# Optimization experiments

Measured on AMD Instinct MI355X. Metric: run time of the kernel, lower is better.

## Reference

```python
import jax, jax.numpy as jnp
import numpy as np

N = 100_000          # nodes
G = 2_000            # graphs
MUL0, MUL1 = 256, 128
DIM = MUL0 + 3 * MUL1  # 640
EPS = 1e-5
SQRT_K0 = 1.0 / np.sqrt(MUL0 + MUL1)          # fan_in of 0e slice: 256+128
SQRT_K1 = 1.0 / np.sqrt(MUL0 + 2 * MUL1)      # fan_in of 1e slice: 256+128+128


def setup_inputs() -> dict:
    key = jax.random.key(0)
    ks = jax.random.split(key, 8)
    x = jax.random.normal(ks[0], (N, DIM), dtype=jnp.float32)
    y = jax.random.normal(ks[1], (N, 4), dtype=jnp.float32)
    batch = jnp.sort(jax.random.randint(ks[2], (N,), 0, G)).astype(jnp.int32)
    # uvw path weights (e3nn internal weights, randn then rescaled by sqrt_k)
    w000 = jax.random.normal(ks[3], (MUL0, 1, MUL0), dtype=jnp.float32) * SQRT_K0
    w110 = jax.random.normal(ks[4], (MUL1, 1, MUL0), dtype=jnp.float32) * SQRT_K0
    w011 = jax.random.normal(ks[5], (MUL0, 1, MUL1), dtype=jnp.float32) * SQRT_K1
    w101 = jax.random.normal(ks[6], (MUL1, 1, MUL1), dtype=jnp.float32) * SQRT_K1
    w111 = jax.random.normal(ks[7], (MUL1, 1, MUL1), dtype=jnp.float32) * SQRT_K1
    bias0 = jnp.zeros((MUL0,), jnp.float32)           # bias on 0e slice
    mean_shift = jnp.ones((MUL0,), jnp.float32)
    affine_weight = jnp.ones((MUL0 + MUL1,), jnp.float32)
    affine_bias = jnp.zeros((MUL0,), jnp.float32)
    return dict(x=x, y=y, w000=w000, w011=w011, w101=w101, w110=w110,
                w111=w111, bias0=bias0, mean_shift=mean_shift,
                affine_weight=affine_weight, affine_bias=affine_bias,
                batch=batch)


def _segment_mean(vals, batch, counts):
    s = jax.ops.segment_sum(vals, batch, num_segments=G)
    return s / counts.reshape((G,) + (1,) * (vals.ndim - 1))


def reference(x, y, w000, w011, w101, w110, w111, bias0, mean_shift,
              affine_weight, affine_bias, batch):
    n = x.shape[0]
    s1 = x[:, :MUL0]                      # [N,256]  0e
    v1 = x[:, MUL0:].reshape(n, MUL1, 3)  # [N,128,3] 1e
    s2 = y[:, :1]                         # [N,1]    0e
    v2 = y[:, 1:].reshape(n, 1, 3)        # [N,1,3]  1e

    inv_sqrt3 = np.float32(1.0 / np.sqrt(3.0))
    # ---- fully connected tensor product (5 uvw paths) ----
    # output 0e slice: path weight sqrt(d_out)=1
    p000 = jnp.einsum('nu,nv,uvw->nw', s1, s2, w000)
    p110 = jnp.einsum('nui,nvi,uvw->nw', v1, v2, w110) * inv_sqrt3
    out0 = p000 + p110 + bias0                          # bias on scalar-even slice
    # output 1e slice: path weight sqrt(3); CG = 1/sqrt(3) (delta) or 1/sqrt(6) (eps)
    p011 = jnp.einsum('nu,nvk,uvw->nwk', s1, v2, w011)  # sqrt3/sqrt3 = 1
    p101 = jnp.einsum('nui,nv,uvw->nwi', v1, s2, w101)
    cross = jnp.cross(v1, v2)                           # [N,128,3]
    p111 = jnp.einsum('nuk,uvw->nwk', cross, w111) * np.float32(1.0 / np.sqrt(2.0))
    out1 = p011 + p101 + p111                           # [N,128,3]

    counts = jnp.maximum(
        jax.ops.segment_sum(jnp.ones((n,), x.dtype), batch, num_segments=G), 1.0)

    # ---- EquivariantGraphNorm (component norm, mean reduce, affine) ----
    # 0e field: per-graph mean shift, then per-graph rms normalization
    f0_mean = _segment_mean(out0, batch, counts)        # [G,256]
    f0 = out0 - f0_mean[batch] * mean_shift
    n0 = _segment_mean(f0 * f0, batch, counts)          # d=1 component norm
    n0 = jax.lax.rsqrt(n0 + EPS) * affine_weight[:MUL0]
    f0 = f0 * n0[batch] + affine_bias

    # 1e field: component norm = mean over the 3 components
    n1 = _segment_mean(jnp.mean(out1 * out1, axis=-1), batch, counts)  # [G,128]
    n1 = jax.lax.rsqrt(n1 + EPS) * affine_weight[MUL0:]
    f1 = out1 * n1[batch][:, :, None]

    return jnp.concatenate([f0, f1.reshape(n, MUL1 * 3)], axis=-1)
```

## Files before the change

kernel.cpp:

```cpp
#include <hip/hip_runtime.h>
#include <math.h>

#define N_ROWS 100000
#define NG     2000
#define M0     256
#define M1     128
#define DIMX   640
#define EPSV   1e-5f
#define BM     32

#define INV_SQRT3 0.57735026918962576f
#define INV_SQRT2 0.70710678118654752f

#define OFF_U  0
#define OFF_D  98304
#define OFF_V  131072
#define WT_TOTAL 163840

typedef __attribute__((ext_vector_type(8))) short bf16x8;
typedef __attribute__((ext_vector_type(4))) float f32x4;

__device__ __forceinline__ unsigned short f2bf(float f) {
    union { float f; unsigned int u; } v; v.f = f;
    unsigned int r = v.u + 0x7fff + ((v.u >> 16) & 1);
    return (unsigned short)(r >> 16);
}
__device__ __forceinline__ float bf2f(unsigned short u) {
    union { unsigned int u; float f; } v; v.u = ((unsigned int)u) << 16; return v.f;
}

__device__ __forceinline__ int lower_bound_i(const int* __restrict__ b, int n, int key) {
    int lo = 0, hi = n;
    while (lo < hi) { int m = (lo + hi) >> 1; if (b[m] < key) lo = m + 1; else hi = m; }
    return lo;
}

__global__ __launch_bounds__(256)
void k0_pack(const float* __restrict__ w000, const float* __restrict__ w011,
             const float* __restrict__ w101, const float* __restrict__ w110,
             const float* __restrict__ w111, unsigned short* __restrict__ WT)
{
    int i = blockIdx.x * 256 + threadIdx.x;
    if (i >= WT_TOTAL) return;
    int l = (i >> 3) & 63, e = i & 7;
    int lc = l & 15, lk = (l >> 4) << 3;
    float val;
    if (i < OFF_D) {
        int tile = i >> 9; int f = tile >> 3, kk = tile & 7;
        int col = f * 16 + lc, k = kk * 32 + lk + e;
        val = (col < 256) ? w000[k * 256 + col] : w011[k * 128 + (col - 256)];
    } else if (i < OFF_V) {
        int j = i - OFF_D; int tile = j >> 9; int f = tile >> 2, kk = tile & 3;
        int col = f * 16 + lc, k = kk * 32 + lk + e;
        val = w110[k * 256 + col] * INV_SQRT3;
    } else {
        int j = i - OFF_V; int tile = j >> 9; int f = tile >> 2, kk = tile & 3;
        int col = f * 16 + lc, k = kk * 32 + lk + e;
        val = (col < 128) ? w101[k * 128 + col]
                          : w111[k * 128 + (col - 128)] * INV_SQRT2;
    }
    WT[i] = f2bf(val);
}

__device__ __forceinline__ bf16x8 ldA(const unsigned short* base, int KW,
                                      int row, int kk, int kg)
{
    int off = row * KW + (((kk << 5) + (kg << 3)) ^ ((row & 7) << 3));
    return *(const bf16x8*)(base + off);
}

__global__ __launch_bounds__(256, 3)
void k1_mfma(const float* __restrict__ x, const float* __restrict__ y,
             const unsigned short* __restrict__ WT, const float* __restrict__ bias0,
             float* __restrict__ out)
{
    __shared__ unsigned short xs1[BM][256];
    __shared__ unsigned short xv[3][BM][128];
    __shared__ unsigned short xd[BM][128];
    __shared__ float sY[BM][4];
    __shared__ float sBias[256];

    const int t    = threadIdx.x;
    const int lane = t & 63;
    const int wv   = t >> 6;
    const int cb   = lane & 15;
    const int kg   = lane >> 4;
    const int hy   = blockIdx.x & 1;
    const int n0   = (blockIdx.x >> 1) * BM;

    if (t < 128) sY[t >> 2][t & 3] = y[(size_t)(n0 + (t >> 2)) * 4 + (t & 3)];
    sBias[t] = bias0[t];

    #pragma unroll
    for (int i = 0; i < 8; ++i) {
        int idx = i * 256 + t;
        int r = idx >> 6, c4 = idx & 63;
        float4 v = *(const float4*)(x + (size_t)(n0 + r) * DIMX + c4 * 4);
        ushort4 o = { f2bf(v.x), f2bf(v.y), f2bf(v.z), f2bf(v.w) };
        *(ushort4*)&xs1[r][(c4 * 4) ^ ((r & 7) << 3)] = o;
    }
    #pragma unroll
    for (int i = 0; i < 4; ++i) {
        int idx = i * 256 + t;
        int r = idx >> 5, q = idx & 31;
        const float* vp = x + (size_t)(n0 + r) * DIMX + M0 + q * 12;
        float4 a = *(const float4*)vp;
        float4 b = *(const float4*)(vp + 4);
        float4 c = *(const float4*)(vp + 8);
        int off = (q * 4) ^ ((r & 7) << 3);
        ushort4 ox = { f2bf(a.x), f2bf(a.w), f2bf(b.z), f2bf(c.y) };
        ushort4 oy = { f2bf(a.y), f2bf(b.x), f2bf(b.w), f2bf(c.z) };
        ushort4 oz = { f2bf(a.z), f2bf(b.y), f2bf(c.x), f2bf(c.w) };
        *(ushort4*)&xv[0][r][off] = ox;
        *(ushort4*)&xv[1][r][off] = oy;
        *(ushort4*)&xv[2][r][off] = oz;
    }
    __syncthreads();

    #pragma unroll
    for (int i = 0; i < 4; ++i) {
        int idx = i * 256 + t;
        int r = idx >> 5, q = idx & 31;
        int off = (q * 4) ^ ((r & 7) << 3);
        ushort4 ux = *(const ushort4*)&xv[0][r][off];
        ushort4 uy = *(const ushort4*)&xv[1][r][off];
        ushort4 uz = *(const ushort4*)&xv[2][r][off];
        float v2x = sY[r][1], v2y = sY[r][2], v2z = sY[r][3];
        ushort4 od;
        od.x = f2bf(bf2f(ux.x) * v2x + bf2f(uy.x) * v2y + bf2f(uz.x) * v2z);
        od.y = f2bf(bf2f(ux.y) * v2x + bf2f(uy.y) * v2y + bf2f(uz.y) * v2z);
        od.z = f2bf(bf2f(ux.z) * v2x + bf2f(uy.z) * v2y + bf2f(uz.z) * v2z);
        od.w = f2bf(bf2f(ux.w) * v2x + bf2f(uy.w) * v2y + bf2f(uz.w) * v2z);
        *(ushort4*)&xd[r][off] = od;
    }
    __syncthreads();

    float s2v[2][4];
    #pragma unroll
    for (int rg = 0; rg < 2; ++rg)
        #pragma unroll
        for (int j = 0; j < 4; ++j)
            s2v[rg][j] = sY[rg * 16 + kg * 4 + j][0];

    f32x4 aO[2][2];
    f32x4 aG[2];
    #pragma unroll
    for (int q = 0; q < 2; ++q) { aO[q][0] = (f32x4){0,0,0,0}; aO[q][1] = (f32x4){0,0,0,0}; }
    aG[0] = (f32x4){0,0,0,0}; aG[1] = (f32x4){0,0,0,0};

    #pragma unroll
    for (int kk = 0; kk < 8; ++kk) {
        bf16x8 a0 = ldA(&xs1[0][0], 256, cb, kk, kg);
        bf16x8 a1 = ldA(&xs1[0][0], 256, 16 + cb, kk, kg);
        #pragma unroll
        for (int q = 0; q < 3; ++q) {
            int f = (q < 2) ? (wv * 4 + hy * 2 + q) : (16 + wv * 2 + hy);
            bf16x8 b = *(const bf16x8*)(WT + OFF_U + (size_t)(f * 8 + kk) * 512 + lane * 8);
            if (q < 2) {
                aO[q][0] = __builtin_amdgcn_mfma_f32_16x16x32_bf16(a0, b, aO[q][0], 0, 0, 0);
                aO[q][1] = __builtin_amdgcn_mfma_f32_16x16x32_bf16(a1, b, aO[q][1], 0, 0, 0);
            } else {
                aG[0] = __builtin_amdgcn_mfma_f32_16x16x32_bf16(a0, b, aG[0], 0, 0, 0);
                aG[1] = __builtin_amdgcn_mfma_f32_16x16x32_bf16(a1, b, aG[1], 0, 0, 0);
            }
        }
    }

    #pragma unroll
    for (int q = 0; q < 2; ++q)
        #pragma unroll
        for (int rg = 0; rg < 2; ++rg)
            #pragma unroll
            for (int j = 0; j < 4; ++j)
                aO[q][rg][j] *= s2v[rg][j];

    #pragma unroll
    for (int kk = 0; kk < 4; ++kk) {
        bf16x8 a0 = ldA(&xd[0][0], 128, cb, kk, kg);
        bf16x8 a1 = ldA(&xd[0][0], 128, 16 + cb, kk, kg);
        #pragma unroll
        for (int q = 0; q < 2; ++q) {
            int f = wv * 4 + hy * 2 + q;
            bf16x8 b = *(const bf16x8*)(WT + OFF_D + (size_t)(f * 4 + kk) * 512 + lane * 8);
            aO[q][0] = __builtin_amdgcn_mfma_f32_16x16x32_bf16(a0, b, aO[q][0], 0, 0, 0);
            aO[q][1] = __builtin_amdgcn_mfma_f32_16x16x32_bf16(a1, b, aO[q][1], 0, 0, 0);
        }
    }

    #pragma unroll
    for (int q = 0; q < 2; ++q) {
        int col = wv * 64 + hy * 32 + q * 16 + cb;
        float bb = sBias[col];
        #pragma unroll
        for (int rg = 0; rg < 2; ++rg)
            #pragma unroll
            for (int j = 0; j < 4; ++j) {
                int row = rg * 16 + kg * 4 + j;
                out[(size_t)(n0 + row) * DIMX + col] = aO[q][rg][j] + bb;
            }
    }

    f32x4 aV[2][3][2];
    #pragma unroll
    for (int q = 0; q < 2; ++q)
        #pragma unroll
        for (int j = 0; j < 3; ++j) { aV[q][j][0] = (f32x4){0,0,0,0}; aV[q][j][1] = (f32x4){0,0,0,0}; }

    #pragma unroll
    for (int kk = 0; kk < 4; ++kk) {
        bf16x8 av[3][2];
        #pragma unroll
        for (int j = 0; j < 3; ++j) {
            av[j][0] = ldA(&xv[j][0][0], 128, cb, kk, kg);
            av[j][1] = ldA(&xv[j][0][0], 128, 16 + cb, kk, kg);
        }
        #pragma unroll
        for (int q = 0; q < 2; ++q) {
            int f = (q == 0) ? (wv * 2 + hy) : (8 + wv * 2 + hy);
            bf16x8 b = *(const bf16x8*)(WT + OFF_V + (size_t)(f * 4 + kk) * 512 + lane * 8);
            #pragma unroll
            for (int j = 0; j < 3; ++j) {
                aV[q][j][0] = __builtin_amdgcn_mfma_f32_16x16x32_bf16(av[j][0], b, aV[q][j][0], 0, 0, 0);
                aV[q][j][1] = __builtin_amdgcn_mfma_f32_16x16x32_bf16(av[j][1], b, aV[q][j][1], 0, 0, 0);
            }
        }
    }

    {
        int w = wv * 32 + hy * 16 + cb;
        #pragma unroll
        for (int rg = 0; rg < 2; ++rg)
            #pragma unroll
            for (int j = 0; j < 4; ++j) {
                int row = rg * 16 + kg * 4 + j;
                int n = n0 + row;
                float g   = aG[rg][j];
                float s2r = sY[row][0];
                float w2x = sY[row][1], w2y = sY[row][2], w2z = sY[row][3];
                float P0 = aV[0][0][rg][j], P1 = aV[0][1][rg][j], P2 = aV[0][2][rg][j];
                float Q0 = aV[1][0][rg][j], Q1 = aV[1][1][rg][j], Q2 = aV[1][2][rg][j];
                float e0 = w2x * g + s2r * P0 + w2z * Q1 - w2y * Q2;
                float e1 = w2y * g + s2r * P1 + w2x * Q2 - w2z * Q0;
                float e2 = w2z * g + s2r * P2 + w2y * Q0 - w2x * Q1;
                float* p = out + (size_t)n * DIMX + M0 + 3 * w;
                *(float2*)p = make_float2(e0, e1);
                p[2] = e2;
            }
    }
}

__global__ __launch_bounds__(384)
void k2_norm(float* __restrict__ out, const int* __restrict__ batch,
             const float* __restrict__ mean_shift, const float* __restrict__ aw,
             const float* __restrict__ ab)
{
    __shared__ int sSE[2];
    const int g = blockIdx.x;
    const int t = threadIdx.x;
    if (t == 0) {
        sSE[0] = lower_bound_i(batch, N_ROWS, g);
        sSE[1] = lower_bound_i(batch, N_ROWS, g + 1);
    }
    __syncthreads();
    const int start = sSE[0], end = sSE[1];
    float cnt = (float)(end - start);
    if (cnt < 1.f) cnt = 1.f;

    if (t < M0) {
        float s = 0.f, q = 0.f;
        for (int n = start; n < end; ++n) {
            float v = out[(size_t)n * DIMX + t];
            s += v;
            q = fmaf(v, v, q);
        }
        float mean = s / cnt;
        float esq  = q / cnt;
        float ms   = mean_shift[t];
        float var  = esq - 2.f * ms * mean * mean + ms * ms * mean * mean;
        float sc   = rsqrtf(var + EPSV) * aw[t];
        float sh   = ab[t] - mean * ms * sc;
        for (int n = start; n < end; ++n) {
            float* p = out + (size_t)n * DIMX + t;
            *p = fmaf(*p, sc, sh);
        }
    } else {
        int w = t - M0;
        float q = 0.f;
        for (int n = start; n < end; ++n) {
            const float* p = out + (size_t)n * DIMX + M0 + w * 3;
            float a = p[0], b = p[1], c = p[2];
            q = fmaf(a, a, q); q = fmaf(b, b, q); q = fmaf(c, c, q);
        }
        float mq = q / (3.f * cnt);
        float sc = rsqrtf(mq + EPSV) * aw[M0 + w];
        for (int n = start; n < end; ++n) {
            float* p = out + (size_t)n * DIMX + M0 + w * 3;
            p[0] *= sc; p[1] *= sc; p[2] *= sc;
        }
    }
}

extern "C" void kernel_launch(void* const* d_in, const int* in_sizes, int n_in,
                              void* d_out, int out_size, void* d_ws, size_t ws_size,
                              hipStream_t stream)
{
    const float* x     = (const float*)d_in[0];
    const float* y     = (const float*)d_in[1];
    const float* w000  = (const float*)d_in[2];
    const float* w011  = (const float*)d_in[3];
    const float* w101  = (const float*)d_in[4];
    const float* w110  = (const float*)d_in[5];
    const float* w111  = (const float*)d_in[6];
    const float* bias0 = (const float*)d_in[7];
    const float* mshift= (const float*)d_in[8];
    const float* aw    = (const float*)d_in[9];
    const float* ab    = (const float*)d_in[10];
    const int*   batch = (const int*)d_in[11];
    float* out = (float*)d_out;

    unsigned short* WT = (unsigned short*)d_ws;

    k0_pack<<<WT_TOTAL / 256, 256, 0, stream>>>(w000, w011, w101, w110, w111, WT);
    k1_mfma<<<(N_ROWS / BM) * 2, 256, 0, stream>>>(x, y, WT, bias0, out);
    k2_norm<<<NG, 384, 0, stream>>>(out, batch, mshift, aw, ab);
}
```

Baseline: 350.7 us.

## Parallelize graph norm across rows with float4 loads and shared-memory reduction

Rewrites the per-graph normalization kernel so 640 threads split into 4 row groups, each reading float4 column chunks, and the partial sums and squares are reduced through shared memory. Per-column scale and shift are precomputed into shared arrays, which lets the apply pass be a single vectorized FMA over all columns, the vector columns included. This replaces the serial per-thread row loops and the strided 3-float accesses, aiming for better memory coalescing and more parallelism. The cost is extra shared memory and block synchronizations.

```diff
diff --git a/kernel.cpp b/kernel.cpp
--- a/kernel.cpp
+++ b/kernel.cpp
@@ -249,12 +249,17 @@
     }
 }
 
-__global__ __launch_bounds__(384)
+__global__ __launch_bounds__(640)
 void k2_norm(float* __restrict__ out, const int* __restrict__ batch,
              const float* __restrict__ mean_shift, const float* __restrict__ aw,
              const float* __restrict__ ab)
 {
-    __shared__ int sSE[2];
+    __shared__ float sS[4][DIMX];
+    __shared__ float sQ[4][DIMX];
+    __shared__ float sScale[DIMX];
+    __shared__ float sShift[DIMX];
+    __shared__ int   sSE[2];
+
     const int g = blockIdx.x;
     const int t = threadIdx.x;
     if (t == 0) {
@@ -266,37 +271,56 @@
     float cnt = (float)(end - start);
     if (cnt < 1.f) cnt = 1.f;
 
+    const int rl = t / 160;
+    const int ct = t % 160;
+    const int c0 = ct * 4;
+
+    float4 s4 = make_float4(0.f, 0.f, 0.f, 0.f);
+    float4 q4 = make_float4(0.f, 0.f, 0.f, 0.f);
+    for (int n = start + rl; n < end; n += 4) {
+        float4 v = *(const float4*)(out + (size_t)n * DIMX + c0);
+        s4.x += v.x; q4.x = fmaf(v.x, v.x, q4.x);
+        s4.y += v.y; q4.y = fmaf(v.y, v.y, q4.y);
+        s4.z += v.z; q4.z = fmaf(v.z, v.z, q4.z);
+        s4.w += v.w; q4.w = fmaf(v.w, v.w, q4.w);
+    }
+    *(float4*)&sS[rl][c0] = s4;
+    *(float4*)&sQ[rl][c0] = q4;
+    __syncthreads();
+
+    float sum = sS[0][t] + sS[1][t] + sS[2][t] + sS[3][t];
+    float sq  = sQ[0][t] + sQ[1][t] + sQ[2][t] + sQ[3][t];
+
     if (t < M0) {
-        float s = 0.f, q = 0.f;
-        for (int n = start; n < end; ++n) {
-            float v = out[(size_t)n * DIMX + t];
-            s += v;
-            q = fmaf(v, v, q);
-        }
-        float mean = s / cnt;
-        float esq  = q / cnt;
+        float mean = sum / cnt;
+        float esq  = sq / cnt;
         float ms   = mean_shift[t];
         float var  = esq - 2.f * ms * mean * mean + ms * ms * mean * mean;
         float sc   = rsqrtf(var + EPSV) * aw[t];
-        float sh   = ab[t] - mean * ms * sc;
-        for (int n = start; n < end; ++n) {
-            float* p = out + (size_t)n * DIMX + t;
-            *p = fmaf(*p, sc, sh);
-        }
+        sScale[t] = sc;
+        sShift[t] = ab[t] - mean * ms * sc;
     } else {
-        int w = t - M0;
-        float q = 0.f;
-        for (int n = start; n < end; ++n) {
-            const float* p = out + (size_t)n * DIMX + M0 + w * 3;
-            float a = p[0], b = p[1], c = p[2];
-            q = fmaf(a, a, q); q = fmaf(b, b, q); q = fmaf(c, c, q);
-        }
-        float mq = q / (3.f * cnt);
-        float sc = rsqrtf(mq + EPSV) * aw[M0 + w];
-        for (int n = start; n < end; ++n) {
-            float* p = out + (size_t)n * DIMX + M0 + w * 3;
-            p[0] *= sc; p[1] *= sc; p[2] *= sc;
-        }
+        sQ[0][t] = sq;
+    }
+    __syncthreads();
+    if (t >= M0) {
+        int w = (t - M0) / 3;
+        float qq = sQ[0][M0 + 3 * w] + sQ[0][M0 + 3 * w + 1] + sQ[0][M0 + 3 * w + 2];
+        sScale[t] = rsqrtf(qq / (3.f * cnt) + EPSV) * aw[M0 + w];
+        sShift[t] = 0.f;
+    }
+    __syncthreads();
+
+    const float4 sc4 = *(const float4*)&sScale[c0];
+    const float4 sh4 = *(const float4*)&sShift[c0];
+    for (int n = start + rl; n < end; n += 4) {
+        float* p = out + (size_t)n * DIMX + c0;
+        float4 v = *(const float4*)p;
+        v.x = fmaf(v.x, sc4.x, sh4.x);
+        v.y = fmaf(v.y, sc4.y, sh4.y);
+        v.z = fmaf(v.z, sc4.z, sh4.z);
+        v.w = fmaf(v.w, sc4.w, sh4.w);
+        *(float4*)p = v;
     }
 }
 
@@ -322,5 +346,5 @@
 
     k0_pack<<<WT_TOTAL / 256, 256, 0, stream>>>(w000, w011, w101, w110, w111, WT);
     k1_mfma<<<(N_ROWS / BM) * 2, 256, 0, stream>>>(x, y, WT, bias0, out);
-    k2_norm<<<NG, 384, 0, stream>>>(out, batch, mshift, aw, ab);
-}
+    k2_norm<<<NG, 640, 0, stream>>>(out, batch, mshift, aw, ab);
+}
```

Result: faster. 326.2 us (-7.0%).

## Fuse graph-norm statistics into GEMM epilogue with atomics and bf16 scratch

Applied to the files above, without the earlier changes.

Per-graph sums and sums of squares are now accumulated inside the MFMA kernel epilogue with atomicAdd into workspace buffers, which removes the separate read passes over the output. A tiny finalize kernel turns these into per-graph scale and shift, and a grid-stride apply kernel normalizes every element in one pass. When the workspace is large enough, the un-normalized result goes to a bf16 scratch buffer to halve the intermediate traffic. The cost is atomic contention, an extra zeroing kernel, and lower precision of the intermediate values that are later normalized.

```diff
diff --git a/kernel.cpp b/kernel.cpp
--- a/kernel.cpp
+++ b/kernel.cpp
@@ -33,6 +33,13 @@
     int lo = 0, hi = n;
     while (lo < hi) { int m = (lo + hi) >> 1; if (b[m] < key) lo = m + 1; else hi = m; }
     return lo;
+}
+
+__global__ __launch_bounds__(256)
+void kz_zero(float* __restrict__ p)
+{
+    int i = blockIdx.x * 256 + threadIdx.x;
+    ((float4*)p)[i] = make_float4(0.f, 0.f, 0.f, 0.f);
 }
 
 __global__ __launch_bounds__(256)
@@ -69,16 +76,21 @@
     return *(const bf16x8*)(base + off);
 }
 
+template<int SCR>
 __global__ __launch_bounds__(256, 3)
 void k1_mfma(const float* __restrict__ x, const float* __restrict__ y,
              const unsigned short* __restrict__ WT, const float* __restrict__ bias0,
-             float* __restrict__ out)
+             const int* __restrict__ batch,
+             float* __restrict__ out, unsigned short* __restrict__ scr,
+             float* __restrict__ wS0, float* __restrict__ wQ0,
+             float* __restrict__ wQ1)
 {
     __shared__ unsigned short xs1[BM][256];
     __shared__ unsigned short xv[3][BM][128];
     __shared__ unsigned short xd[BM][128];
     __shared__ float sY[BM][4];
     __shared__ float sBias[256];
+    __shared__ int   sG[BM];
 
     const int t    = threadIdx.x;
     const int lane = t & 63;
@@ -89,6 +101,7 @@
     const int n0   = (blockIdx.x >> 1) * BM;
 
     if (t < 128) sY[t >> 2][t & 3] = y[(size_t)(n0 + (t >> 2)) * 4 + (t & 3)];
+    if (t < BM)  sG[t] = batch[n0 + t];
     sBias[t] = bias0[t];
 
     #pragma unroll
@@ -196,8 +209,39 @@
             #pragma unroll
             for (int j = 0; j < 4; ++j) {
                 int row = rg * 16 + kg * 4 + j;
-                out[(size_t)(n0 + row) * DIMX + col] = aO[q][rg][j] + bb;
-            }
+                float vv = aO[q][rg][j] + bb;
+                if (SCR) scr[(size_t)(n0 + row) * DIMX + col] = f2bf(vv);
+                else     out[(size_t)(n0 + row) * DIMX + col] = vv;
+            }
+    }
+
+    #pragma unroll
+    for (int q = 0; q < 2; ++q) {
+        int col = wv * 64 + hy * 32 + q * 16 + cb;
+        float bb = sBias[col];
+        #pragma unroll
+        for (int rg = 0; rg < 2; ++rg) {
+            int br = rg * 16 + kg * 4;
+            int g0 = sG[br], g3 = sG[br + 3];
+            if (g0 == g3) {
+                float s = 0.f, qq = 0.f;
+                #pragma unroll
+                for (int j = 0; j < 4; ++j) {
+                    float v = aO[q][rg][j] + bb;
+                    s += v; qq = fmaf(v, v, qq);
+                }
+                atomicAdd(&wS0[g0 * M0 + col], s);
+                atomicAdd(&wQ0[g0 * M0 + col], qq);
+            } else {
+                #pragma unroll
+                for (int j = 0; j < 4; ++j) {
+                    int g = sG[br + j];
+                    float v = aO[q][rg][j] + bb;
+                    atomicAdd(&wS0[g * M0 + col], v);
+                    atomicAdd(&wQ0[g * M0 + col], v * v);
+                }
+            }
+        }
     }
 
     f32x4 aV[2][3][2];
@@ -229,10 +273,13 @@
     {
         int w = wv * 32 + hy * 16 + cb;
         #pragma unroll
-        for (int rg = 0; rg < 2; ++rg)
+        for (int rg = 0; rg < 2; ++rg) {
+            int br = rg * 16 + kg * 4;
+            int g0 = sG[br], g3 = sG[br + 3];
+            float qrun = 0.f;
             #pragma unroll
             for (int j = 0; j < 4; ++j) {
-                int row = rg * 16 + kg * 4 + j;
+                int row = br + j;
                 int n = n0 + row;
                 float g   = aG[rg][j];
                 float s2r = sY[row][0];
@@ -242,17 +289,28 @@
                 float e0 = w2x * g + s2r * P0 + w2z * Q1 - w2y * Q2;
                 float e1 = w2y * g + s2r * P1 + w2x * Q2 - w2z * Q0;
                 float e2 = w2z * g + s2r * P2 + w2y * Q0 - w2x * Q1;
-                float* p = out + (size_t)n * DIMX + M0 + 3 * w;
-                *(float2*)p = make_float2(e0, e1);
-                p[2] = e2;
-            }
+                if (SCR) {
+                    unsigned short* sp = scr + (size_t)n * DIMX + M0 + 3 * w;
+                    sp[0] = f2bf(e0); sp[1] = f2bf(e1); sp[2] = f2bf(e2);
+                } else {
+                    float* p = out + (size_t)n * DIMX + M0 + 3 * w;
+                    *(float2*)p = make_float2(e0, e1);
+                    p[2] = e2;
+                }
+                float esq = e0 * e0 + e1 * e1 + e2 * e2;
+                if (g0 == g3) qrun += esq;
+                else atomicAdd(&wQ1[sG[row] * M1 + w], esq);
+            }
+            if (g0 == g3) atomicAdd(&wQ1[g0 * M1 + w], qrun);
+        }
     }
 }
 
 __global__ __launch_bounds__(384)
-void k2_norm(float* __restrict__ out, const int* __restrict__ batch,
-             const float* __restrict__ mean_shift, const float* __restrict__ aw,
-             const float* __restrict__ ab)
+void k2f_final(const int* __restrict__ batch, const float* __restrict__ mshift,
+               const float* __restrict__ aw, const float* __restrict__ ab,
+               float* __restrict__ wS0, float* __restrict__ wQ0,
+               float* __restrict__ wQ1)
 {
     __shared__ int sSE[2];
     const int g = blockIdx.x;
@@ -262,41 +320,64 @@
         sSE[1] = lower_bound_i(batch, N_ROWS, g + 1);
     }
     __syncthreads();
-    const int start = sSE[0], end = sSE[1];
-    float cnt = (float)(end - start);
+    float cnt = (float)(sSE[1] - sSE[0]);
     if (cnt < 1.f) cnt = 1.f;
 
     if (t < M0) {
-        float s = 0.f, q = 0.f;
-        for (int n = start; n < end; ++n) {
-            float v = out[(size_t)n * DIMX + t];
-            s += v;
-            q = fmaf(v, v, q);
-        }
-        float mean = s / cnt;
-        float esq  = q / cnt;
-        float ms   = mean_shift[t];
+        float sum = wS0[g * M0 + t];
+        float sq  = wQ0[g * M0 + t];
+        float mean = sum / cnt;
+        float esq  = sq / cnt;
+        float ms   = mshift[t];
         float var  = esq - 2.f * ms * mean * mean + ms * ms * mean * mean;
         float sc   = rsqrtf(var + EPSV) * aw[t];
-        float sh   = ab[t] - mean * ms * sc;
-        for (int n = start; n < end; ++n) {
-            float* p = out + (size_t)n * DIMX + t;
-            *p = fmaf(*p, sc, sh);
-        }
+        wS0[g * M0 + t] = sc;
+        wQ0[g * M0 + t] = ab[t] - mean * ms * sc;
     } else {
         int w = t - M0;
-        float q = 0.f;
-        for (int n = start; n < end; ++n) {
-            const float* p = out + (size_t)n * DIMX + M0 + w * 3;
-            float a = p[0], b = p[1], c = p[2];
-            q = fmaf(a, a, q); q = fmaf(b, b, q); q = fmaf(c, c, q);
-        }
-        float mq = q / (3.f * cnt);
-        float sc = rsqrtf(mq + EPSV) * aw[M0 + w];
-        for (int n = start; n < end; ++n) {
-            float* p = out + (size_t)n * DIMX + M0 + w * 3;
-            p[0] *= sc; p[1] *= sc; p[2] *= sc;
-        }
+        float qq = wQ1[g * M1 + w];
+        wQ1[g * M1 + w] = rsqrtf(qq / (3.f * cnt) + EPSV) * aw[M0 + w];
+    }
+}
+
+template<int SCR>
+__global__ __launch_bounds__(256)
+void k3_apply(float* __restrict__ out, const unsigned short* __restrict__ scr,
+              const int* __restrict__ batch, const float* __restrict__ A0,
+              const float* __restrict__ B0, const float* __restrict__ A1)
+{
+    const int total4 = N_ROWS * DIMX / 4;
+    for (int idx = blockIdx.x * 256 + threadIdx.x; idx < total4; idx += gridDim.x * 256) {
+        int n  = idx / (DIMX / 4);
+        int c4 = idx - n * (DIMX / 4);
+        int c  = c4 * 4;
+        int g  = batch[n];
+
+        float4 v;
+        if (SCR) {
+            ushort4 u = *(const ushort4*)(scr + (size_t)n * DIMX + c);
+            v = make_float4(bf2f(u.x), bf2f(u.y), bf2f(u.z), bf2f(u.w));
+        } else {
+            v = ((float4*)out)[idx];
+        }
+        if (c < M0) {
+            float4 a = *(const float4*)(A0 + g * M0 + c);
+            float4 b = *(const float4*)(B0 + g * M0 + c);
+            v.x = fmaf(v.x, a.x, b.x);
+            v.y = fmaf(v.y, a.y, b.y);
+            v.z = fmaf(v.z, a.z, b.z);
+            v.w = fmaf(v.w, a.w, b.w);
+        } else {
+            int e = c - M0;
+            float r[4] = { v.x, v.y, v.z, v.w };
+            #pragma unroll
+            for (int j = 0; j < 4; ++j) {
+                int w = (e + j) / 3;
+                r[j] *= A1[g * M1 + w];
+            }
+            v = make_float4(r[0], r[1], r[2], r[3]);
+        }
+        ((float4*)out)[idx] = v;
     }
 }
 
@@ -319,8 +400,28 @@
     float* out = (float*)d_out;
 
     unsigned short* WT = (unsigned short*)d_ws;
-
+    float* wS0 = (float*)((char*)d_ws + WT_TOTAL * 2);
+    float* wQ0 = wS0 + NG * M0;
+    float* wQ1 = wQ0 + NG * M0;
+    unsigned short* scr = (unsigned short*)(wQ1 + NG * M1);
+
+    const size_t need_scr = (size_t)WT_TOTAL * 2 + (size_t)NG * (M0 + M0 + M1) * 4
+                          + (size_t)N_ROWS * DIMX * 2;
+    const bool use_scr = ws_size >= need_scr;
+
+    kz_zero<<<1250, 256, 0, stream>>>(wS0);
     k0_pack<<<WT_TOTAL / 256, 256, 0, stream>>>(w000, w011, w101, w110, w111, WT);
-    k1_mfma<<<(N_ROWS / BM) * 2, 256, 0, stream>>>(x, y, WT, bias0, out);
-    k2_norm<<<NG, 384, 0, stream>>>(out, batch, mshift, aw, ab);
-}
+    if (use_scr) {
+        k1_mfma<1><<<(N_ROWS / BM) * 2, 256, 0, stream>>>(x, y, WT, bias0, batch,
+                                                          out, scr, wS0, wQ0, wQ1);
+    } else {
+        k1_mfma<0><<<(N_ROWS / BM) * 2, 256, 0, stream>>>(x, y, WT, bias0, batch,
+                                                          out, scr, wS0, wQ0, wQ1);
+    }
+    k2f_final<<<NG, 384, 0, stream>>>(batch, mshift, aw, ab, wS0, wQ0, wQ1);
+    if (use_scr) {
+        k3_apply<1><<<2048, 256, 0, stream>>>(out, scr, batch, wS0, wQ0, wQ1);
+    } else {
+        k3_apply<0><<<2048, 256, 0, stream>>>(out, scr, batch, wS0, wQ0, wQ1);
+    }
+}
```

After: 358.4 us. 2.2% more time.
